# Kernel optimization log

Measured on AMD Instinct MI355X. Metric: run time of the kernel, lower is better.

## Reference

```python
import jax, jax.numpy as jnp
import numpy as np


def _rel_index(h):
    # static relative-position index for an h x h grid (torch meshgrid 'ij')
    coords = np.stack(np.meshgrid(np.arange(h), np.arange(h), indexing='ij'))  # (2,h,h)
    cf = coords.reshape(2, -1)                       # (2, N)
    rel = cf[:, :, None] - cf[:, None, :]            # (2, N, N)
    rel = rel.transpose(1, 2, 0)                     # (N, N, 2)
    rel[..., 0] += h - 1
    rel[..., 1] += h - 1
    rel[..., 0] *= 2 * h - 1
    return rel.sum(-1)                               # (N, N) int


def _conv2d_s2(x, w, b):
    y = jax.lax.conv_general_dilated(x, w, window_strides=(2, 2),
                                     padding=[(1, 1), (1, 1)],
                                     dimension_numbers=('NCHW', 'OIHW', 'NCHW'))
    return y + b[None, :, None, None]


def _attn(z, qkv_w, qkv_b, out_w, out_b, table, heads):
    # H == reduce_size for every layer in this config, so no interp of K/V.
    B, C, H, W = z.shape
    N = H * W
    inner = qkv_w.shape[0] // 3
    d = inner // heads
    qkv = jnp.einsum('oc,bchw->bohw', qkv_w, z) + qkv_b[None, :, None, None]
    q, k, v = jnp.split(qkv, 3, axis=1)
    # channel layout is (dim_head, heads) with heads fastest (einops '(dim_head heads)')
    def split_heads(t):
        return t.reshape(B, d, heads, N).transpose(0, 2, 3, 1)  # b h n d
    q, k, v = split_heads(q), split_heads(k), split_heads(v)
    att = jnp.einsum('bhid,bhjd->bhij', q, k)
    idx = _rel_index(H)
    bias = table[idx.reshape(-1)].reshape(N, N, heads).transpose(2, 0, 1)  # (h, N, N)
    att = (att + bias[None]) * (d ** -0.5)  # bias added BEFORE scale, as in source
    att = jax.nn.softmax(att, axis=-1)
    o = jnp.einsum('bhij,bhjd->bhid', att, v)
    o = o.transpose(0, 3, 1, 2).reshape(B, d * heads, H, W)  # back to (dim_head heads) layout
    return jnp.einsum('oc,bchw->bohw', out_w, o) + out_b[None, :, None, None]


def setup_inputs() -> dict:
    key = jax.random.key(0)
    ks = jax.random.split(key, 24)
    heads = 3
    dims = [16, 32, 64]
    in_chs = [1, 16, 32]
    reds = [32, 16, 8]
    inp = {'x': jax.random.normal(ks[0], (32, 1, 64, 64), dtype=jnp.float32)}
    j = 1
    for i, (dim, cin, r) in enumerate(zip(dims, in_chs, reds), start=1):
        dh = dim // heads
        inner = dh * heads
        inp[f'conv{i}_w'] = jax.random.normal(ks[j], (dim, cin, 3, 3), dtype=jnp.float32) * 0.05; j += 1
        inp[f'conv{i}_b'] = jax.random.normal(ks[j], (dim,), dtype=jnp.float32) * 0.01; j += 1
        inp[f'qkv{i}_w'] = jax.random.normal(ks[j], (inner * 3, dim), dtype=jnp.float32) * 0.05; j += 1
        inp[f'qkv{i}_b'] = jax.random.normal(ks[j], (inner * 3,), dtype=jnp.float32) * 0.01; j += 1
        inp[f'out{i}_w'] = jax.random.normal(ks[j], (dim, inner), dtype=jnp.float32) * 0.05; j += 1
        inp[f'out{i}_b'] = jax.random.normal(ks[j], (dim,), dtype=jnp.float32) * 0.01; j += 1
        inp[f'rel{i}'] = jax.random.normal(ks[j], ((2 * r - 1) * (2 * r - 1), heads), dtype=jnp.float32) * 0.02; j += 1
    inp['cls_w'] = jax.random.normal(ks[j], (10, 64), dtype=jnp.float32) * 0.05; j += 1
    inp['cls_b'] = jax.random.normal(ks[j], (10,), dtype=jnp.float32) * 0.01
    return inp


def reference(x, conv1_w, conv1_b, qkv1_w, qkv1_b, out1_w, out1_b, rel1,
              conv2_w, conv2_b, qkv2_w, qkv2_b, out2_w, out2_b, rel2,
              conv3_w, conv3_b, qkv3_w, qkv3_b, out3_w, out3_b, rel3,
              cls_w, cls_b):
    heads = 3
    z = jax.nn.relu(_conv2d_s2(x, conv1_w, conv1_b))
    z = _attn(z, qkv1_w, qkv1_b, out1_w, out1_b, rel1, heads) + z
    z = jax.nn.relu(_conv2d_s2(z, conv2_w, conv2_b))
    z = _attn(z, qkv2_w, qkv2_b, out2_w, out2_b, rel2, heads) + z
    z = jax.nn.relu(_conv2d_s2(z, conv3_w, conv3_b))
    z = _attn(z, qkv3_w, qkv3_b, out3_w, out3_b, rel3, heads) + z
    z = z.mean(axis=(2, 3))           # adaptive avg pool to 1x1 + flatten -> (B, 64)
    cls_output = z @ cls_w.T + cls_b  # CLS_head linear (dropout inactive in eval)
    return (z, cls_output)
```

## Files before the change

kernel.cpp:

```cpp
#include <hip/hip_runtime.h>
#include <math.h>

#define CDIV(a, b) (((a) + (b) - 1) / (b))

#define LOG2E 1.4426950408889634f
#define SC5  (0.44721359549996f * LOG2E)
#define SC10 (0.31622776601684f * LOG2E)
#define SC21 (0.21821789023599f * LOG2E)
#define EXP2(x) __builtin_amdgcn_exp2f(x)

template <int N> __device__ inline void waitcnt_vm() {
    if constexpr (N == 0) asm volatile("s_waitcnt vmcnt(0)" ::: "memory");
    else if constexpr (N == 2) asm volatile("s_waitcnt vmcnt(2)" ::: "memory");
    else if constexpr (N == 3) asm volatile("s_waitcnt vmcnt(3)" ::: "memory");
    else if constexpr (N == 4) asm volatile("s_waitcnt vmcnt(4)" ::: "memory");
    else if constexpr (N == 6) asm volatile("s_waitcnt vmcnt(6)" ::: "memory");
    else static_assert(N < 0, "unsupported vmcnt literal");
}

template <int CIN, int HIN, int COUT, int HOUT, int INNER, int DP, int KVRS, int KVD, int TPX>
__global__ void __launch_bounds__(256) conv_qkv(const float* __restrict__ in,
                                                const float* __restrict__ cw,
                                                const float* __restrict__ cb,
                                                const float* __restrict__ qw,
                                                const float* __restrict__ qb,
                                                float* __restrict__ z, float* __restrict__ q,
                                                float* __restrict__ kv) {
    constexpr int N = HOUT * HOUT;
    __shared__ float zt[COUT * TPX];
    const int b  = blockIdx.x / (N / TPX);
    const int n0 = (blockIdx.x % (N / TPX)) * TPX;
    const int tid = threadIdx.x;

    for (int idx = tid; idx < COUT * TPX; idx += 256) {
        int c = idx / TPX, px = idx % TPX;
        int n = n0 + px;
        int ho = n / HOUT, wo = n % HOUT;
        float acc = cb[c];
        for (int ci = 0; ci < CIN; ++ci) {
            const float* ip = in + (size_t)(b * CIN + ci) * HIN * HIN;
            const float* wp = cw + (size_t)(c * CIN + ci) * 9;
            #pragma unroll
            for (int kh = 0; kh < 3; ++kh) {
                int hi = 2 * ho + kh - 1;
                if (hi < 0 || hi >= HIN) continue;
                #pragma unroll
                for (int kw = 0; kw < 3; ++kw) {
                    int wi = 2 * wo + kw - 1;
                    if (wi < 0 || wi >= HIN) continue;
                    acc = fmaf(wp[kh * 3 + kw], ip[hi * HIN + wi], acc);
                }
            }
        }
        acc = fmaxf(acc, 0.f);
        zt[idx] = acc;
        z[((size_t)(b * COUT) + c) * N + n] = acc;
    }
    __syncthreads();

    constexpr int OC3 = 3 * INNER;
    for (int idx = tid; idx < OC3 * TPX; idx += 256) {
        int oc = idx / TPX, px = idx % TPX;
        float val = qb[oc];
        const float* wp = qw + (size_t)oc * COUT;
        #pragma unroll 8
        for (int c = 0; c < COUT; ++c) val = fmaf(wp[c], zt[c * TPX + px], val);
        int part = oc / INNER;
        int r = oc - part * INNER;
        int hh = r % 3, dd = r / 3;
        size_t n = n0 + px;
        if (part == 0)
            q[((size_t)(b * 3 + hh) * N + n) * DP + dd] = val;
        else
            kv[((size_t)(b * 3 + hh) * N + n) * KVRS + (part - 1) * KVD + dd] = val;
    }
}

template <int CPREV, int INNERP, int DPREV, int HINW, int COUT, int HOUT, int INNER, int DP,
          int KVRS, int KVD, int TPX>
__global__ void __launch_bounds__(256) fused_oc(const float* __restrict__ o1,
                                                const float* __restrict__ ow,
                                                const float* __restrict__ ob,
                                                const float* __restrict__ zres,
                                                const float* __restrict__ cw,
                                                const float* __restrict__ cb,
                                                const float* __restrict__ qw,
                                                const float* __restrict__ qb,
                                                float* __restrict__ z, float* __restrict__ q,
                                                float* __restrict__ kv) {
    constexpr int N2 = HOUT * HOUT;
    constexpr int N1 = HINW * HINW;
    constexpr int TROWS = TPX / HOUT;
    constexpr int HR = 2 * TROWS + 1;
    constexpr int HALO = HR * HINW;
    __shared__ float smem[INNERP * HALO + CPREV * HALO];
    float* o1s = smem;
    float* zh  = smem + INNERP * HALO;
    float* zt  = smem;
    const int b  = blockIdx.x / (N2 / TPX);
    const int n0 = (blockIdx.x % (N2 / TPX)) * TPX;
    const int tid = threadIdx.x;
    const int ho0 = n0 / HOUT;
    const int row0 = 2 * ho0 - 1;

    for (int t = tid; t < INNERP * HALO; t += 256) {
        int hd = t / HALO, p = t - hd * HALO;
        int row = row0 + p / HINW;
        float v = 0.f;
        if (row >= 0 && row < HINW)
            v = o1[((size_t)(b * INNERP + hd)) * N1 + row * HINW + (p % HINW)];
        o1s[t] = v;
    }
    __syncthreads();

    for (int t = tid; t < CPREV * HALO; t += 256) {
        int ci = t / HALO, p = t - ci * HALO;
        int row = row0 + p / HINW;
        float val = 0.f;
        if (row >= 0 && row < HINW) {
            int n1 = row * HINW + (p % HINW);
            val = ob[ci] + zres[((size_t)(b * CPREV) + ci) * N1 + n1];
            const float* wp = ow + (size_t)ci * INNERP;
            for (int dd = 0; dd < DPREV; ++dd) {
                #pragma unroll
                for (int hh = 0; hh < 3; ++hh)
                    val = fmaf(wp[dd * 3 + hh], o1s[(hh * DPREV + dd) * HALO + p], val);
            }
        }
        zh[t] = val;
    }
    __syncthreads();

    for (int idx = tid; idx < COUT * TPX; idx += 256) {
        int c = idx / TPX, px = idx - (idx / TPX) * TPX;
        int hol = px / HOUT, wo = px - hol * HOUT;
        float acc = cb[c];
        for (int ci = 0; ci < CPREV; ++ci) {
            const float* zp = zh + ci * HALO;
            const float* wp = cw + (size_t)(c * CPREV + ci) * 9;
            #pragma unroll
            for (int kh = 0; kh < 3; ++kh) {
                int r = 2 * hol + kh;
                #pragma unroll
                for (int kw = 0; kw < 3; ++kw) {
                    int col = 2 * wo + kw - 1;
                    if (col < 0 || col >= HINW) continue;
                    acc = fmaf(wp[kh * 3 + kw], zp[r * HINW + col], acc);
                }
            }
        }
        acc = fmaxf(acc, 0.f);
        zt[idx] = acc;
        z[((size_t)(b * COUT) + c) * N2 + n0 + px] = acc;
    }
    __syncthreads();

    constexpr int OC3 = 3 * INNER;
    for (int idx = tid; idx < OC3 * TPX; idx += 256) {
        int oc = idx / TPX, px = idx % TPX;
        float val = qb[oc];
        const float* wp = qw + (size_t)oc * COUT;
        #pragma unroll 8
        for (int c = 0; c < COUT; ++c) val = fmaf(wp[c], zt[c * TPX + px], val);
        int part = oc / INNER;
        int r = oc - part * INNER;
        int hh = r % 3, dd = r / 3;
        size_t n = n0 + px;
        if (part == 0)
            q[((size_t)(b * 3 + hh) * N2 + n) * DP + dd] = val;
        else
            kv[((size_t)(b * 3 + hh) * N2 + n) * KVRS + (part - 1) * KVD + dd] = val;
    }
}

template <int D, int QP, int RS, int RPT, int TILE, int NW>
__global__ void __launch_bounds__(NW * 64) attn_big(const float* __restrict__ q,
                                                    const float* __restrict__ kv,
                                                    const float* __restrict__ table,
                                                    float* __restrict__ o, int N, int log2Hg,
                                                    int T, float scale2) {
    extern __shared__ float smem[];
    float* tb = smem;
    float* comb = smem;
    constexpr int BT = NW * 64;
    constexpr int ROWS = 64 * RPT;
    constexpr int CSTR = (D % 2 == 0) ? (D + 3) : (D + 2);
    constexpr int RV4 = RS / 4;
    constexpr int TBYTES = TILE * RS * 4;
    constexpr int LPT = CDIV(TBYTES, 1024);
    constexpr bool FULLT = (TBYTES % 1024) == 0;
    static_assert(LPT == 3, "vmcnt literal below assumes 3 loads per tile");

    const int bh = blockIdx.x % 96;
    const int chunk = blockIdx.x / 96;
    const int h = bh % 3;
    const int tid = threadIdx.x;
    const int wave = tid >> 6;
    const int lane = tid & 63;
    const int Hg = 1 << log2Hg;
    const int W2 = 2 * Hg - 1;
    const int base = chunk * ROWS;

    float* kvw = smem + ((T + 3) & ~3) + wave * (2 * TILE * RS);

    for (int t = tid; t < T; t += BT) tb[t] = table[t * 3 + h] * scale2;

    float qr[RPT][D];
    const float* tbp[RPT];
    #pragma unroll
    for (int r = 0; r < RPT; ++r) {
        int i = base + lane + 64 * r;
        const float* qg = q + ((size_t)bh * N + i) * QP;
        #pragma unroll
        for (int dd = 0; dd < D; ++dd) qr[r][dd] = qg[dd];
        tbp[r] = tb + (((i >> log2Hg) + Hg - 1) * W2 + (i & (Hg - 1)) + Hg - 1);
    }

    float acc[RPT][D];
    float lsum[RPT];
    #pragma unroll
    for (int r = 0; r < RPT; ++r) {
        lsum[r] = 0.f;
        #pragma unroll
        for (int dd = 0; dd < D; ++dd) acc[r][dd] = 0.f;
    }

    const float* kvbase = kv + (size_t)bh * N * RS;
    const int NJ = N / NW;
    const int NT = NJ / TILE;
    const int j0 = wave * NJ;

    auto stage = [&](int bufIdx, int t) {
        const float* srcf = kvbase + (size_t)(j0 + t * TILE) * RS;
        float* dstf = kvw + bufIdx * (TILE * RS);
        #pragma unroll
        for (int x = 0; x < LPT; ++x) {
            if (FULLT || (x * 1024 + lane * 16) < TBYTES) {
                const void* g = (const void*)(srcf + x * 256 + lane * 4);
                void* l = (void*)(dstf + x * 256);
                __builtin_amdgcn_global_load_lds(
                    (const __attribute__((address_space(1))) void*)g,
                    (__attribute__((address_space(3))) void*)l, 16, 0, 0);
            }
        }
    };

    stage(0, 0);
    if (NT > 1) stage(1, 1);

    __syncthreads();

    for (int t = 0; t < NT; ++t) {
        const float* curb = kvw + (t & 1) * (TILE * RS);
        const int jt = j0 + t * TILE;
        for (int jg = 0; jg < TILE; jg += 4) {
            #pragma unroll
            for (int k = 0; k < 4; ++k) {
                const int j = jt + jg + k;
                const float* kr = curb + (jg + k) * RS;
                const int joff = (j >> log2Hg) * W2 + (j & (Hg - 1));
                #pragma unroll
                for (int r = 0; r < RPT; ++r) {
                    float s = 0.f;
                    #pragma unroll
                    for (int dd = 0; dd < D; ++dd) s = fmaf(qr[r][dd], kr[dd], s);
                    float e = EXP2(fmaf(s, scale2, tbp[r][-joff]));
                    lsum[r] += e;
                    #pragma unroll
                    for (int dd = 0; dd < D; ++dd) acc[r][dd] = fmaf(e, kr[D + dd], acc[r][dd]);
                }
            }
        }
        if (t + 2 < NT) {
            asm volatile("s_waitcnt lgkmcnt(0)" ::: "memory");
            stage(t & 1, t + 2);
            waitcnt_vm<3>();
        } else if (t + 1 < NT) {
            waitcnt_vm<0>();
        }
    }

    for (int half = NW / 2; half >= 1; half >>= 1) {
        __syncthreads();
        if (wave >= half && wave < 2 * half) {
            #pragma unroll
            for (int r = 0; r < RPT; ++r) {
                float* cp = comb + (size_t)((wave - half) * ROWS + lane + 64 * r) * CSTR;
                #pragma unroll
                for (int dd = 0; dd < D; ++dd) cp[dd] = acc[r][dd];
                cp[D] = lsum[r];
            }
        }
        __syncthreads();
        if (wave < half) {
            #pragma unroll
            for (int r = 0; r < RPT; ++r) {
                const float* cp = comb + (size_t)(wave * ROWS + lane + 64 * r) * CSTR;
                #pragma unroll
                for (int dd = 0; dd < D; ++dd) acc[r][dd] += cp[dd];
                lsum[r] += cp[D];
            }
        }
    }
    if (wave == 0) {
        #pragma unroll
        for (int r = 0; r < RPT; ++r) {
            float inv = 1.0f / lsum[r];
            int i = base + lane + 64 * r;
            #pragma unroll
            for (int dd = 0; dd < D; ++dd)
                o[((size_t)bh * D + dd) * N + i] = acc[r][dd] * inv;
        }
    }
}

__global__ void __launch_bounds__(256) attn_small(const float* __restrict__ q,
                                                  const float* __restrict__ kv,
                                                  const float* __restrict__ table,
                                                  float* __restrict__ o, float scale2) {
    constexpr int D = 21, DP = 24, NN = 64;
    constexpr int CSTR = 23;
    __shared__ float smem[4 * NN * CSTR];
    float* kvs = smem;
    float* tb = kvs + NN * 2 * DP;
    float* comb = smem;

    const int bh = blockIdx.x;
    const int h = bh % 3;
    const int tid = threadIdx.x;
    const int wave = tid >> 6;
    const int lane = tid & 63;

    {
        const float4* kvg = (const float4*)(kv + (size_t)bh * NN * 2 * DP);
        float4* kvs4 = (float4*)kvs;
        for (int t = tid; t < NN * 2 * DP / 4; t += 256) kvs4[t] = kvg[t];
        for (int t = tid; t < 225; t += 256) tb[t] = table[t * 3 + h] * scale2;
    }

    const int i = lane;
    const float* qg = q + ((size_t)bh * NN + i) * DP;
    float qr[D];
    #pragma unroll
    for (int dd = 0; dd < D; ++dd) qr[dd] = qg[dd];
    const int ibase = ((i >> 3) + 7) * 15 + (i & 7) + 7;
    __syncthreads();

    float acc[D];
    #pragma unroll
    for (int dd = 0; dd < D; ++dd) acc[dd] = 0.f;
    float lsum = 0.f;

    const int j0 = wave * 16;
    #pragma unroll
    for (int jj = 0; jj < 16; ++jj) {
        const int j = j0 + jj;
        float4 r4[12];
        const float4* rp = (const float4*)(kvs + j * 2 * DP);
        #pragma unroll
        for (int x = 0; x < 12; ++x) r4[x] = rp[x];
        const float* kr = (const float*)r4;
        const float* vr = kr + DP;
        const int joff = (j >> 3) * 15 + (j & 7);
        float s = 0.f;
        #pragma unroll
        for (int dd = 0; dd < D; ++dd) s = fmaf(qr[dd], kr[dd], s);
        float e = EXP2(fmaf(s, scale2, tb[ibase - joff]));
        lsum += e;
        #pragma unroll
        for (int dd = 0; dd < D; ++dd) acc[dd] = fmaf(e, vr[dd], acc[dd]);
    }

    __syncthreads();
    {
        float* cp = comb + (size_t)(wave * NN + lane) * CSTR;
        #pragma unroll
        for (int dd = 0; dd < D; ++dd) cp[dd] = acc[dd];
        cp[D] = lsum;
    }
    __syncthreads();
    if (tid < NN) {
        float af[D];
        #pragma unroll
        for (int dd = 0; dd < D; ++dd) af[dd] = 0.f;
        float lf = 0.f;
        #pragma unroll
        for (int wv = 0; wv < 4; ++wv) {
            const float* cp = comb + (size_t)(wv * NN + tid) * CSTR;
            #pragma unroll
            for (int dd = 0; dd < D; ++dd) af[dd] += cp[dd];
            lf += cp[D];
        }
        float inv = 1.0f / lf;
        #pragma unroll
        for (int dd = 0; dd < D; ++dd)
            o[((size_t)bh * D + dd) * NN + tid] = af[dd] * inv;
    }
}

__global__ void __launch_bounds__(256) tail(const float* __restrict__ o,
                                            const float* __restrict__ ow,
                                            const float* __restrict__ ob,
                                            const float* __restrict__ zin,
                                            const float* __restrict__ cw,
                                            const float* __restrict__ cb,
                                            float* __restrict__ out) {
    __shared__ float os[63 * 64];
    __shared__ float zt[64 * 65];
    __shared__ float p[64];
    const int b = blockIdx.x;
    const int tid = threadIdx.x;
    for (int t = tid; t < 63 * 64; t += 256) os[t] = o[(size_t)(b * 63) * 64 + t];
    __syncthreads();
    for (int idx = tid; idx < 64 * 64; idx += 256) {
        int c = idx >> 6, n = idx & 63;
        float val = ob[c] + zin[((size_t)(b * 64) + c) * 64 + n];
        const float* wp = ow + (size_t)c * 63;
        for (int dd = 0; dd < 21; ++dd) {
            #pragma unroll
            for (int hh = 0; hh < 3; ++hh)
                val = fmaf(wp[dd * 3 + hh], os[(hh * 21 + dd) * 64 + n], val);
        }
        zt[c * 65 + n] = val;
    }
    __syncthreads();
    if (tid < 64) {
        float s = 0.f;
        #pragma unroll
        for (int n = 0; n < 64; ++n) s += zt[tid * 65 + n];
        s *= (1.0f / 64.0f);
        p[tid] = s;
        out[b * 64 + tid] = s;
    }
    __syncthreads();
    if (tid < 10) {
        float val = cb[tid];
        const float* wp = cw + (size_t)tid * 64;
        #pragma unroll
        for (int kk = 0; kk < 64; ++kk) val = fmaf(wp[kk], p[kk], val);
        out[2048 + b * 10 + tid] = val;
    }
}

extern "C" void kernel_launch(void* const* d_in, const int* in_sizes, int n_in,
                              void* d_out, int out_size, void* d_ws, size_t ws_size,
                              hipStream_t stream) {
    float* ws = (float*)d_ws;
    float* Zc1 = ws;
    float* Zc2 = Zc1 + 524288;
    float* Q   = Zc2 + 262144;
    float* KV  = Q + 786432;
    float* O   = KV + 1572864;

    float* out = (float*)d_out;

    conv_qkv<1, 64, 16, 32, 15, 8, 12, 5, 32><<<32 * 32, 256, 0, stream>>>(
        (const float*)d_in[0], (const float*)d_in[1], (const float*)d_in[2],
        (const float*)d_in[3], (const float*)d_in[4], Zc1, Q, KV);
    attn_big<5, 8, 12, 8, 64, 8><<<96 * 2, 512, 65040, stream>>>(
        Q, KV, (const float*)d_in[7], O, 1024, 5, 3969, SC5);

    fused_oc<16, 15, 5, 32, 32, 16, 30, 12, 20, 10, 16><<<32 * 16, 256, 0, stream>>>(
        O, (const float*)d_in[5], (const float*)d_in[6], Zc1,
        (const float*)d_in[8], (const float*)d_in[9],
        (const float*)d_in[10], (const float*)d_in[11], Zc2, Q, KV);
    attn_big<10, 12, 20, 1, 32, 8><<<96 * 4, 512, 44816, stream>>>(
        Q, KV, (const float*)d_in[14], O, 256, 4, 961, SC10);

    fused_oc<32, 30, 10, 16, 64, 8, 63, 24, 48, 24, 8><<<32 * 8, 256, 0, stream>>>(
        O, (const float*)d_in[12], (const float*)d_in[13], Zc2,
        (const float*)d_in[15], (const float*)d_in[16],
        (const float*)d_in[17], (const float*)d_in[18], Zc1, Q, KV);
    attn_small<<<96, 256, 0, stream>>>(Q, KV, (const float*)d_in[21], O, SC21);

    tail<<<32, 256, 0, stream>>>(
        O, (const float*)d_in[19], (const float*)d_in[20], Zc1,
        (const float*)d_in[22], (const float*)d_in[23], out);
}
```

Measured before the change: 283.7 us.

## Software-pipeline K/V and bias LDS reads in layer-1 attention, retile grid

Adds a compile-time group size G to the big attention kernel. When G > 0, each group of K/V rows and relative-bias values is read from LDS into registers one group ahead of the compute that uses it, using vector loads, so LDS latency overlaps with the FMA and exp2 work. The layer-1 launch is also retiled from 8 rows per thread and 8 waves over 192 blocks to 2 rows per thread and 4 waves over 768 blocks, with less shared memory per block. This raises parallelism and occupancy, but costs extra registers for the double-buffered values and more redundant K/V staging across blocks.

```diff
diff --git a/kernel.cpp b/kernel.cpp
--- a/kernel.cpp
+++ b/kernel.cpp
@@ -173,7 +173,7 @@
     }
 }
 
-template <int D, int QP, int RS, int RPT, int TILE, int NW>
+template <int D, int QP, int RS, int RPT, int TILE, int NW, int G>
 __global__ void __launch_bounds__(NW * 64) attn_big(const float* __restrict__ q,
                                                     const float* __restrict__ kv,
                                                     const float* __restrict__ table,
@@ -253,24 +253,81 @@
     for (int t = 0; t < NT; ++t) {
         const float* curb = kvw + (t & 1) * (TILE * RS);
         const int jt = j0 + t * TILE;
-        for (int jg = 0; jg < TILE; jg += 4) {
-            #pragma unroll
-            for (int k = 0; k < 4; ++k) {
-                const int j = jt + jg + k;
-                const float* kr = curb + (jg + k) * RS;
+
+        if constexpr (G > 0) {
+            static_assert(D == 5 && RS == 12 && TILE % G == 0, "pipeline assumes L1 shape");
+            constexpr int NGR = TILE / G;
+            float4 gka[2][G], gkb[2][G];
+            float2 gkc[2][G];
+            float  gtb[2][G][RPT];
+            #pragma unroll
+            for (int k = 0; k < G; ++k) {
+                const float* rp = curb + k * RS;
+                gka[0][k] = *(const float4*)rp;
+                gkb[0][k] = *(const float4*)(rp + 4);
+                gkc[0][k] = *(const float2*)(rp + 8);
+                const int j = jt + k;
                 const int joff = (j >> log2Hg) * W2 + (j & (Hg - 1));
                 #pragma unroll
-                for (int r = 0; r < RPT; ++r) {
-                    float s = 0.f;
+                for (int r = 0; r < RPT; ++r) gtb[0][k][r] = tbp[r][-joff];
+            }
+            #pragma unroll
+            for (int g = 0; g < NGR; ++g) {
+                const int cur = g & 1, nxt = cur ^ 1;
+                if (g + 1 < NGR) {
                     #pragma unroll
-                    for (int dd = 0; dd < D; ++dd) s = fmaf(qr[r][dd], kr[dd], s);
-                    float e = EXP2(fmaf(s, scale2, tbp[r][-joff]));
-                    lsum[r] += e;
+                    for (int k = 0; k < G; ++k) {
+                        const float* rp = curb + ((g + 1) * G + k) * RS;
+                        gka[nxt][k] = *(const float4*)rp;
+                        gkb[nxt][k] = *(const float4*)(rp + 4);
+                        gkc[nxt][k] = *(const float2*)(rp + 8);
+                        const int j = jt + (g + 1) * G + k;
+                        const int joff = (j >> log2Hg) * W2 + (j & (Hg - 1));
+                        #pragma unroll
+                        for (int r = 0; r < RPT; ++r) gtb[nxt][k][r] = tbp[r][-joff];
+                    }
+                }
+                #pragma unroll
+                for (int k = 0; k < G; ++k) {
+                    const float kf[10] = {gka[cur][k].x, gka[cur][k].y, gka[cur][k].z,
+                                          gka[cur][k].w, gkb[cur][k].x, gkb[cur][k].y,
+                                          gkb[cur][k].z, gkb[cur][k].w, gkc[cur][k].x,
+                                          gkc[cur][k].y};
                     #pragma unroll
-                    for (int dd = 0; dd < D; ++dd) acc[r][dd] = fmaf(e, kr[D + dd], acc[r][dd]);
+                    for (int r = 0; r < RPT; ++r) {
+                        float s = 0.f;
+                        #pragma unroll
+                        for (int dd = 0; dd < D; ++dd) s = fmaf(qr[r][dd], kf[dd], s);
+                        float e = EXP2(fmaf(s, scale2, gtb[cur][k][r]));
+                        lsum[r] += e;
+                        #pragma unroll
+                        for (int dd = 0; dd < D; ++dd)
+                            acc[r][dd] = fmaf(e, kf[D + dd], acc[r][dd]);
+                    }
                 }
             }
-        }
+        } else {
+            for (int jg = 0; jg < TILE; jg += 4) {
+                #pragma unroll
+                for (int k = 0; k < 4; ++k) {
+                    const int j = jt + jg + k;
+                    const float* kr = curb + (jg + k) * RS;
+                    const int joff = (j >> log2Hg) * W2 + (j & (Hg - 1));
+                    #pragma unroll
+                    for (int r = 0; r < RPT; ++r) {
+                        float s = 0.f;
+                        #pragma unroll
+                        for (int dd = 0; dd < D; ++dd) s = fmaf(qr[r][dd], kr[dd], s);
+                        float e = EXP2(fmaf(s, scale2, tbp[r][-joff]));
+                        lsum[r] += e;
+                        #pragma unroll
+                        for (int dd = 0; dd < D; ++dd)
+                            acc[r][dd] = fmaf(e, kr[D + dd], acc[r][dd]);
+                    }
+                }
+            }
+        }
+
         if (t + 2 < NT) {
             asm volatile("s_waitcnt lgkmcnt(0)" ::: "memory");
             stage(t & 1, t + 2);
@@ -457,14 +514,14 @@
     conv_qkv<1, 64, 16, 32, 15, 8, 12, 5, 32><<<32 * 32, 256, 0, stream>>>(
         (const float*)d_in[0], (const float*)d_in[1], (const float*)d_in[2],
         (const float*)d_in[3], (const float*)d_in[4], Zc1, Q, KV);
-    attn_big<5, 8, 12, 8, 64, 8><<<96 * 2, 512, 65040, stream>>>(
+    attn_big<5, 8, 12, 2, 64, 4, 4><<<96 * 8, 256, 40464, stream>>>(
         Q, KV, (const float*)d_in[7], O, 1024, 5, 3969, SC5);
 
     fused_oc<16, 15, 5, 32, 32, 16, 30, 12, 20, 10, 16><<<32 * 16, 256, 0, stream>>>(
         O, (const float*)d_in[5], (const float*)d_in[6], Zc1,
         (const float*)d_in[8], (const float*)d_in[9],
         (const float*)d_in[10], (const float*)d_in[11], Zc2, Q, KV);
-    attn_big<10, 12, 20, 1, 32, 8><<<96 * 4, 512, 44816, stream>>>(
+    attn_big<10, 12, 20, 1, 32, 8, 0><<<96 * 4, 512, 44816, stream>>>(
         Q, KV, (const float*)d_in[14], O, 256, 4, 961, SC10);
 
     fused_oc<32, 30, 10, 16, 64, 8, 63, 24, 48, 24, 8><<<32 * 8, 256, 0, stream>>>(
```

Measured after the change: 687.4 us. 2.42x slower.
